# Optimization experiments

Measured on AMD Instinct MI355X. Metric: run time of the kernel, lower is better.

The kernel has to match this reference:

```python
import jax, jax.numpy as jnp
import numpy as np

OUT, IN = 4096, 4096
GROUP_SIZE = 128
NUMEL = OUT * IN                 # 16,777,216 int4 values
N_GROUPS = NUMEL // GROUP_SIZE   # 131,072
N_PACKED = NUMEL // 2            # 8,388,608 bytes (stored as int32 0..255)


def _dequantize_int4(q_packed, q_scales, q_zeros):
    """Unpack two 4-bit values per byte, dequant per group, reshape to (OUT, IN)."""
    low = q_packed & 0xF                     # [N_PACKED]
    high = (q_packed >> 4) & 0xF             # [N_PACKED]
    # interleave: flat[2i] = low nibble, flat[2i+1] = high nibble
    q = jnp.stack([low, high], axis=-1).reshape(NUMEL)            # [NUMEL] int
    qg = q.astype(jnp.float32).reshape(N_GROUPS, GROUP_SIZE)      # [G, group]
    w = (qg - q_zeros[:, None]) * q_scales[:, None]
    return w.reshape(OUT, IN)


def setup_inputs() -> dict:
    key = jax.random.key(0)
    k = jax.random.split(key, 6)
    x = jax.random.normal(k[0], (4, 2048, IN), dtype=jnp.float32)
    q_packed = jax.random.randint(k[1], (N_PACKED,), 0, 256, dtype=jnp.int32)
    q_scales = jax.random.uniform(k[2], (N_GROUPS,), dtype=jnp.float32) * 0.02 + 1e-3
    q_zeros = jax.random.uniform(k[3], (N_GROUPS,), dtype=jnp.float32) * 15.0
    delta_weight = jax.random.normal(k[4], (OUT, IN), dtype=jnp.float32) * 0.01
    bias = jax.random.normal(k[5], (OUT,), dtype=jnp.float32)
    return {"x": x, "q_packed": q_packed, "q_scales": q_scales,
            "q_zeros": q_zeros, "delta_weight": delta_weight, "bias": bias}


def reference(x, q_packed, q_scales, q_zeros, delta_weight, bias):
    W = _dequantize_int4(q_packed, q_scales, q_zeros)   # [OUT, IN]
    W_eff = W + delta_weight
    # F.linear: y = x @ W_eff^T + bias
    h = jnp.einsum('bsi,oi->bso', x, W_eff) + bias
    return h
```

## Files before the change

kernel.cpp:

```cpp
#include <hip/hip_runtime.h>


#define M_DIM 8192
#define N_DIM 4096
#define K_DIM 4096
#define NUMEL (N_DIM * K_DIM)

typedef _Float16 half_t;
typedef __attribute__((ext_vector_type(4))) _Float16 half4v;
typedef __attribute__((ext_vector_type(8))) _Float16 half8v;
typedef __attribute__((ext_vector_type(4))) float float4v;
typedef __attribute__((ext_vector_type(4))) int int4v;

#define KTILES 64
#define LDT 72

static __device__ __forceinline__ void gload16(const void* g, void* l) {
    __builtin_amdgcn_global_load_lds(
        (const __attribute__((address_space(1))) void*)g,
        (__attribute__((address_space(3))) void*)l, 16, 0, 0);
}

__global__ __launch_bounds__(256) void k_pack_w(
    const int* __restrict__ qp, const float* __restrict__ sc,
    const float* __restrict__ zr, const float* __restrict__ dwt,
    unsigned char* __restrict__ Wp)
{
    const size_t o = ((size_t)blockIdx.x * 256 + threadIdx.x) << 4;
    const int chunk16 = (int)(o >> 14);
    const int c  = (int)(o >> 10) & 15;
    const int ln = (int)(o >> 4) & 63;
    const int n = (chunk16 >> 6) * 128 + (c >> 1) * 16 + (ln & 15);
    const int k = (chunk16 & 63) * 64 + (c & 1) * 32 + (ln >> 4) * 8;
    const long flat = (long)n * K_DIM + k;
    const int g = n * 32 + (k >> 7);
    const float s = sc[g];
    const float zs = zr[g] * s;
    int4v q4 = *(const int4v*)(qp + (flat >> 1));
    float4v d0 = *(const float4v*)(dwt + flat);
    float4v d1 = *(const float4v*)(dwt + flat + 4);
    float d[8] = {d0[0], d0[1], d0[2], d0[3], d1[0], d1[1], d1[2], d1[3]};
    half8v vh;
#pragma unroll
    for (int j = 0; j < 4; ++j) {
        vh[2*j]   = (half_t)fmaf((float)(q4[j] & 15),        s, d[2*j]   - zs);
        vh[2*j+1] = (half_t)fmaf((float)((q4[j] >> 4) & 15), s, d[2*j+1] - zs);
    }
    *(half8v*)(Wp + o) = vh;
}

__global__ __launch_bounds__(256) void k_pack_x(
    const float* __restrict__ X, unsigned char* __restrict__ Xp)
{
    const size_t o = ((size_t)blockIdx.x * 256 + threadIdx.x) << 4;
    const int chunk16 = (int)(o >> 14);
    const int c  = (int)(o >> 10) & 15;
    const int ln = (int)(o >> 4) & 63;
    const int m = (chunk16 >> 6) * 128 + (c >> 1) * 16 + (ln & 15);
    const int k = (chunk16 & 63) * 64 + (c & 1) * 32 + (ln >> 4) * 8;
    const float* src = X + (size_t)m * K_DIM + k;
    float4v x0 = *(const float4v*)(src);
    float4v x1 = *(const float4v*)(src + 4);
    half8v vh;
    vh[0] = (half_t)x0[0]; vh[1] = (half_t)x0[1];
    vh[2] = (half_t)x0[2]; vh[3] = (half_t)x0[3];
    vh[4] = (half_t)x1[0]; vh[5] = (half_t)x1[1];
    vh[6] = (half_t)x1[2]; vh[7] = (half_t)x1[3];
    *(half8v*)(Xp + o) = vh;
}

#define BARX() do { __builtin_amdgcn_sched_barrier(0); \
                    __builtin_amdgcn_s_barrier(); \
                    __builtin_amdgcn_sched_barrier(0); } while(0)
#define WAITV0() do { __builtin_amdgcn_sched_barrier(0); \
                      asm volatile("s_waitcnt vmcnt(0)" ::: "memory"); \
                      __builtin_amdgcn_sched_barrier(0); } while(0)

#define STAGE_TILE(BUF, T) do { \
    const int kt_ = (T) >> 1; \
    const size_t ko_ = ((size_t)kt_ << 14) + (((T) & 1) << 10) + choff; \
    gload16(Apk + apan0 + ko_, &lds[BUF][ldsd]); \
    gload16(Apk + apan1 + ko_, &lds[BUF][ldsd + 8192]); \
    gload16(Bpk + bpan0 + ko_, &lds[BUF][ldsd + 16384]); \
    gload16(Bpk + bpan1 + ko_, &lds[BUF][ldsd + 24576]); \
} while(0)

#define RD_A(BUF, DST, RT0) do { \
_Pragma("unroll") for (int i_ = 0; i_ < 4; ++i_) \
        DST[i_] = *(const half8v*)(&lds[BUF][awm + (((RT0) + i_) << 10) + lane16]); \
} while(0)

#define RD_B(BUF, DST) do { \
_Pragma("unroll") for (int j_ = 0; j_ < 4; ++j_) \
        DST[j_] = *(const half8v*)(&lds[BUF][16384 + bq + (j_ << 10) + lane16]); \
} while(0)

#define MFMA16(A0, AR, BR) do { \
    __builtin_amdgcn_s_setprio(1); \
_Pragma("unroll") for (int i_ = 0; i_ < 4; ++i_) \
_Pragma("unroll") for (int j_ = 0; j_ < 4; ++j_) \
        acc[(A0)+i_][j_] = __builtin_amdgcn_mfma_f32_16x16x32_f16( \
            AR[i_], BR[j_], acc[(A0)+i_][j_], 0, 0, 0); \
    __builtin_amdgcn_s_setprio(0); \
} while(0)

#define WINDOW(BA, BB, TA, STG) do { \
    if (STG) { STAGE_TILE((BA)^2, (TA)+2); STAGE_TILE((BB)^2, (TA)+3); } \
    RD_A(BA, ahA, 0); RD_B(BA, bfA); \
    MFMA16(0, ahA, bfA); \
    RD_A(BA, ah2, 4); \
    MFMA16(4, ah2, bfA); \
    RD_A(BB, ahB, 0); RD_B(BB, bfB); \
    MFMA16(0, ahB, bfB); \
    RD_A(BB, ah2, 4); \
    MFMA16(4, ah2, bfB); \
    WAITV0(); BARX(); \
} while(0)

__global__ __launch_bounds__(512, 2) void k_gemm_win(
    const unsigned char* __restrict__ Apk, const unsigned char* __restrict__ Bpk,
    const float* __restrict__ bias, float* __restrict__ Y)
{
    __shared__ __align__(16) unsigned char lds[4][32768];

    const int tid  = threadIdx.x;
    const int lane = tid & 63;
    const int wave = tid >> 6;
    const int wm = wave >> 2;
    const int wn = wave & 3;
    const int awm = wm * 8192;
    const int bq  = (wn >> 1) * 8192 + (wn & 1) * 4096;
    const int lane16 = lane << 4;
    const int ldsd = tid << 4;
    const size_t choff = ((size_t)(tid >> 6) << 11) + ((tid & 63) << 4);

    const int wg = blockIdx.x;
    const int swg = (wg & 7) * 64 + (wg >> 3);
    const int bn = swg & 15;
    const int bm = swg >> 4;

    const size_t apan0 = ((size_t)(2 * bm) * KTILES) << 14;
    const size_t apan1 = ((size_t)(2 * bm + 1) * KTILES) << 14;
    const size_t bpan0 = ((size_t)(2 * bn) * KTILES) << 14;
    const size_t bpan1 = ((size_t)(2 * bn + 1) * KTILES) << 14;

    half8v ahA[4], ahB[4], ah2[4], bfA[4], bfB[4];
    float4v acc[8][4];
    const float4v zero4 = {0.f, 0.f, 0.f, 0.f};
#pragma unroll
    for (int i = 0; i < 8; ++i)
#pragma unroll
        for (int j = 0; j < 4; ++j) acc[i][j] = zero4;

    STAGE_TILE(0, 0); STAGE_TILE(1, 1);
    WAITV0();
    BARX();

    for (int it = 0; it < 31; ++it) {
        const int t = it << 2;
        WINDOW(0, 1, t, 1);
        WINDOW(2, 3, t + 2, 1);
    }
    WINDOW(0, 1, 124, 1);
    WINDOW(2, 3, 126, 0);

    const long m0 = (long)bm * 256 + wm * 128;
    const long n0 = (long)bn * 256 + wn * 64;
#pragma unroll
    for (int mf = 0; mf < 8; ++mf) {
        const long row = m0 + mf * 16 + (lane >> 4) * 4;
#pragma unroll
        for (int nf = 0; nf < 4; ++nf) {
            const long col = n0 + nf * 16 + (lane & 15);
            const float b = bias[col];
#pragma unroll
            for (int r = 0; r < 4; ++r)
                __builtin_nontemporal_store(acc[mf][nf][r] + b,
                                            &Y[(row + r) * N_DIM + col]);
        }
    }
}

__global__ __launch_bounds__(256, 2) void k_gemm_fused(
    const float* __restrict__ X, const int* __restrict__ qp,
    const float* __restrict__ sc, const float* __restrict__ zr,
    const float* __restrict__ dwt,
    const float* __restrict__ bias, float* __restrict__ Y)
{
    __shared__ __align__(16) half_t Ah[128 * LDT];
    __shared__ __align__(16) half_t Bh[128 * LDT];

    const int tid  = threadIdx.x;
    const int lane = tid & 63;
    const int wave = tid >> 6;
    const int wm = wave >> 1, wn = wave & 1;
    const int bn = blockIdx.x & 31;
    const int bm = blockIdx.x >> 5;
    const long m0 = (long)bm * 128;
    const long n0 = (long)bn * 128;
    const int fr = lane & 15;
    const int ko = (lane >> 4) * 8;

    const float4v zero4 = {0.f, 0.f, 0.f, 0.f};
    float4v acc[4][4];
#pragma unroll
    for (int i = 0; i < 4; ++i)
#pragma unroll
        for (int j = 0; j < 4; ++j) acc[i][j] = zero4;

    for (int k0 = 0; k0 < K_DIM; k0 += 64) {
        {
            const int ar = tid >> 4;
            const int ac = (tid & 15) * 4;
#pragma unroll
            for (int rr = 0; rr < 8; ++rr) {
                const int row = ar + rr * 16;
                float4v xv = *(const float4v*)(X + (m0 + row) * K_DIM + k0 + ac);
                half4v h;
#pragma unroll
                for (int j = 0; j < 4; ++j) h[j] = (half_t)xv[j];
                *(half4v*)(Ah + row * LDT + ac) = h;
            }
        }
        {
            const int cr = tid >> 3;
            const int cc = (tid & 7) * 8;
#pragma unroll
            for (int rr = 0; rr < 4; ++rr) {
                const int row = cr + rr * 32;
                const long n = n0 + row;
                const int g = (int)(n * 32 + (k0 >> 7));
                const float s = sc[g];
                const float zs = zr[g] * s;
                const long flat = n * K_DIM + k0 + cc;
                int4v q4 = *(const int4v*)(qp + (flat >> 1));
                float4v d0 = *(const float4v*)(dwt + flat);
                float4v d1 = *(const float4v*)(dwt + flat + 4);
                float d[8] = {d0[0], d0[1], d0[2], d0[3], d1[0], d1[1], d1[2], d1[3]};
                half8v vh;
#pragma unroll
                for (int j = 0; j < 4; ++j) {
                    vh[2*j]   = (half_t)fmaf((float)(q4[j] & 15),        s, d[2*j]   - zs);
                    vh[2*j+1] = (half_t)fmaf((float)((q4[j] >> 4) & 15), s, d[2*j+1] - zs);
                }
                *(half8v*)(Bh + row * LDT + cc) = vh;
            }
        }
        __syncthreads();
#pragma unroll
        for (int ks = 0; ks < 2; ++ks) {
            const int kk = ks * 32 + ko;
            half8v a2[4], b2[4];
#pragma unroll
            for (int i = 0; i < 4; ++i) {
                a2[i] = *(const half8v*)(Ah + (wm * 64 + i * 16 + fr) * LDT + kk);
                b2[i] = *(const half8v*)(Bh + (wn * 64 + i * 16 + fr) * LDT + kk);
            }
#pragma unroll
            for (int i = 0; i < 4; ++i)
#pragma unroll
                for (int j = 0; j < 4; ++j)
                    acc[i][j] = __builtin_amdgcn_mfma_f32_16x16x32_f16(
                        a2[i], b2[j], acc[i][j], 0, 0, 0);
        }
        __syncthreads();
    }

#pragma unroll
    for (int i = 0; i < 4; ++i) {
        const long mrow = m0 + wm * 64 + i * 16 + (lane >> 4) * 4;
#pragma unroll
        for (int j = 0; j < 4; ++j) {
            const long col = n0 + wn * 64 + j * 16 + (lane & 15);
            const float b = bias[col];
#pragma unroll
            for (int r = 0; r < 4; ++r)
                Y[(mrow + r) * N_DIM + col] = acc[i][j][r] + b;
        }
    }
}

extern "C" void kernel_launch(void* const* d_in, const int* in_sizes, int n_in,
                              void* d_out, int out_size, void* d_ws, size_t ws_size,
                              hipStream_t stream)
{
    const float* X  = (const float*)d_in[0];
    const int*   qp = (const int*)d_in[1];
    const float* sc = (const float*)d_in[2];
    const float* zr = (const float*)d_in[3];
    const float* dwt = (const float*)d_in[4];
    const float* bs = (const float*)d_in[5];
    float* Y = (float*)d_out;

    const size_t needB = (size_t)N_DIM * K_DIM * 2;
    const size_t needA = (size_t)M_DIM * K_DIM * 2;

    if (ws_size >= needA + needB) {
        unsigned char* Bpk = (unsigned char*)d_ws;
        unsigned char* Apk = Bpk + needB;
        k_pack_w<<<dim3((unsigned)(needB >> 12)), dim3(256), 0, stream>>>(qp, sc, zr, dwt, Bpk);
        k_pack_x<<<dim3((unsigned)(needA >> 12)), dim3(256), 0, stream>>>(X, Apk);
        k_gemm_win<<<dim3((M_DIM / 256) * (N_DIM / 256)), dim3(512), 0, stream>>>(Apk, Bpk, bs, Y);
    } else {
        k_gemm_fused<<<dim3((M_DIM / 128) * (N_DIM / 128)), dim3(256), 0, stream>>>(
            X, qp, sc, zr, dwt, bs, Y);
    }
}
```

Baseline: 302.4 us.

## Shrink GEMM tile to 128x256 with triple-buffered LDS for higher occupancy

Replaces the 256x256-tile windowed GEMM with a 128x256 tile that uses three 24KB LDS buffers and half the accumulators, launching twice as many workgroups with a target of 4 blocks per CU. The pipeline now issues the next tile's loads after reading fragments and waits with a partial vmcnt, so loads overlap the MFMAs. The smaller tile is meant to lower register and LDS pressure so more waves can hide latency. In exchange each tile reuses A and B less, global traffic per FLOP goes up, and the output stores drop the nontemporal hint.

Result: no change. 305.6 us (+1.1%).

```diff
diff --git a/kernel.cpp b/kernel.cpp
--- a/kernel.cpp
+++ b/kernel.cpp
@@ -72,111 +72,110 @@
 #define BARX() do { __builtin_amdgcn_sched_barrier(0); \
                     __builtin_amdgcn_s_barrier(); \
                     __builtin_amdgcn_sched_barrier(0); } while(0)
-#define WAITV0() do { __builtin_amdgcn_sched_barrier(0); \
-                      asm volatile("s_waitcnt vmcnt(0)" ::: "memory"); \
+#define WAITV(N) do { asm volatile("s_waitcnt vmcnt(" #N ")" ::: "memory"); \
                       __builtin_amdgcn_sched_barrier(0); } while(0)
-
-#define STAGE_TILE(BUF, T) do { \
-    const int kt_ = (T) >> 1; \
-    const size_t ko_ = ((size_t)kt_ << 14) + (((T) & 1) << 10) + choff; \
-    gload16(Apk + apan0 + ko_, &lds[BUF][ldsd]); \
-    gload16(Apk + apan1 + ko_, &lds[BUF][ldsd + 8192]); \
-    gload16(Bpk + bpan0 + ko_, &lds[BUF][ldsd + 16384]); \
-    gload16(Bpk + bpan1 + ko_, &lds[BUF][ldsd + 24576]); \
+#define LGKM0() do { asm volatile("s_waitcnt lgkmcnt(0)" ::: "memory"); \
+                     __builtin_amdgcn_sched_barrier(0); } while(0)
+
+#define STAGE(BUF, T) do { \
+    const size_t ko_ = ((size_t)((T) >> 1) << 14) + (size_t)(((T) & 1) << 10); \
+    gload16(aB + ko_,  &lds[BUF][sdst]); \
+    gload16(bB0 + ko_, &lds[BUF][sdst + 8192]); \
+    gload16(bB1 + ko_, &lds[BUF][sdst + 16384]); \
 } while(0)
 
-#define RD_A(BUF, DST, RT0) do { \
+#define RD_AB(BUF) do { \
 _Pragma("unroll") for (int i_ = 0; i_ < 4; ++i_) \
-        DST[i_] = *(const half8v*)(&lds[BUF][awm + (((RT0) + i_) << 10) + lane16]); \
+        ah[i_] = *(const half8v*)(&lds[BUF][aoff + (i_ << 10)]); \
+_Pragma("unroll") for (int j_ = 0; j_ < 4; ++j_) \
+        bh[j_] = *(const half8v*)(&lds[BUF][boff + (j_ << 10)]); \
 } while(0)
 
-#define RD_B(BUF, DST) do { \
-_Pragma("unroll") for (int j_ = 0; j_ < 4; ++j_) \
-        DST[j_] = *(const half8v*)(&lds[BUF][16384 + bq + (j_ << 10) + lane16]); \
-} while(0)
-
-#define MFMA16(A0, AR, BR) do { \
+#define MFMA16() do { \
     __builtin_amdgcn_s_setprio(1); \
 _Pragma("unroll") for (int i_ = 0; i_ < 4; ++i_) \
 _Pragma("unroll") for (int j_ = 0; j_ < 4; ++j_) \
-        acc[(A0)+i_][j_] = __builtin_amdgcn_mfma_f32_16x16x32_f16( \
-            AR[i_], BR[j_], acc[(A0)+i_][j_], 0, 0, 0); \
+        acc[i_][j_] = __builtin_amdgcn_mfma_f32_16x16x32_f16( \
+            ah[i_], bh[j_], acc[i_][j_], 0, 0, 0); \
     __builtin_amdgcn_s_setprio(0); \
 } while(0)
 
-#define WINDOW(BA, BB, TA, STG) do { \
-    if (STG) { STAGE_TILE((BA)^2, (TA)+2); STAGE_TILE((BB)^2, (TA)+3); } \
-    RD_A(BA, ahA, 0); RD_B(BA, bfA); \
-    MFMA16(0, ahA, bfA); \
-    RD_A(BA, ah2, 4); \
-    MFMA16(4, ah2, bfA); \
-    RD_A(BB, ahB, 0); RD_B(BB, bfB); \
-    MFMA16(0, ahB, bfB); \
-    RD_A(BB, ah2, 4); \
-    MFMA16(4, ah2, bfB); \
-    WAITV0(); BARX(); \
+#define STEP(RB, SB, T) do { \
+    RD_AB(RB); \
+    STAGE(SB, (T) + 2); \
+    WAITV(3); \
+    LGKM0(); \
+    BARX(); \
+    MFMA16(); \
 } while(0)
 
-__global__ __launch_bounds__(512, 2) void k_gemm_win(
+__global__ __launch_bounds__(512, 4) void k_gemm_occ(
     const unsigned char* __restrict__ Apk, const unsigned char* __restrict__ Bpk,
     const float* __restrict__ bias, float* __restrict__ Y)
 {
-    __shared__ __align__(16) unsigned char lds[4][32768];
+    __shared__ __align__(16) unsigned char lds[3][24576];
 
     const int tid  = threadIdx.x;
     const int lane = tid & 63;
     const int wave = tid >> 6;
-    const int wm = wave >> 2;
-    const int wn = wave & 3;
-    const int awm = wm * 8192;
-    const int bq  = (wn >> 1) * 8192 + (wn & 1) * 4096;
+    const int wm2 = wave >> 2;
+    const int wn2 = wave & 3;
     const int lane16 = lane << 4;
-    const int ldsd = tid << 4;
-    const size_t choff = ((size_t)(tid >> 6) << 11) + ((tid & 63) << 4);
+    const int aoff = (wm2 << 12) + lane16;
+    const int boff = 8192 + ((wn2 >> 1) << 13) + ((wn2 & 1) << 12) + lane16;
+    const int sdst = tid << 4;
 
     const int wg = blockIdx.x;
-    const int swg = (wg & 7) * 64 + (wg >> 3);
+    const int swg = (wg & 7) * 128 + (wg >> 3);
     const int bn = swg & 15;
     const int bm = swg >> 4;
 
-    const size_t apan0 = ((size_t)(2 * bm) * KTILES) << 14;
-    const size_t apan1 = ((size_t)(2 * bm + 1) * KTILES) << 14;
-    const size_t bpan0 = ((size_t)(2 * bn) * KTILES) << 14;
-    const size_t bpan1 = ((size_t)(2 * bn + 1) * KTILES) << 14;
-
-    half8v ahA[4], ahB[4], ah2[4], bfA[4], bfB[4];
-    float4v acc[8][4];
+    const size_t thoff = ((size_t)(tid >> 6) << 11) + (size_t)((tid & 63) << 4);
+    const unsigned char* aB  = Apk + ((size_t)bm << 20) + thoff;
+    const unsigned char* bB0 = Bpk + ((size_t)(2 * bn) << 20) + thoff;
+    const unsigned char* bB1 = Bpk + ((size_t)(2 * bn + 1) << 20) + thoff;
+
+    half8v ah[4], bh[4];
+    float4v acc[4][4];
     const float4v zero4 = {0.f, 0.f, 0.f, 0.f};
 #pragma unroll
-    for (int i = 0; i < 8; ++i)
+    for (int i = 0; i < 4; ++i)
 #pragma unroll
         for (int j = 0; j < 4; ++j) acc[i][j] = zero4;
 
-    STAGE_TILE(0, 0); STAGE_TILE(1, 1);
-    WAITV0();
+    STAGE(0, 0);
+    STAGE(1, 1);
+    WAITV(3);
     BARX();
 
-    for (int it = 0; it < 31; ++it) {
-        const int t = it << 2;
-        WINDOW(0, 1, t, 1);
-        WINDOW(2, 3, t + 2, 1);
-    }
-    WINDOW(0, 1, 124, 1);
-    WINDOW(2, 3, 126, 0);
-
-    const long m0 = (long)bm * 256 + wm * 128;
-    const long n0 = (long)bn * 256 + wn * 64;
-#pragma unroll
-    for (int mf = 0; mf < 8; ++mf) {
-        const long row = m0 + mf * 16 + (lane >> 4) * 4;
-#pragma unroll
-        for (int nf = 0; nf < 4; ++nf) {
-            const long col = n0 + nf * 16 + (lane & 15);
+    for (int it = 0; it < 42; ++it) {
+        const int t = it * 3;
+        STEP(0, 2, t);
+        STEP(1, 0, t + 1);
+        STEP(2, 1, t + 2);
+    }
+
+    RD_AB(0);
+    WAITV(0);
+    LGKM0();
+    BARX();
+    MFMA16();
+    RD_AB(1);
+    LGKM0();
+    MFMA16();
+
+    const long m0 = (long)bm * 128 + wm2 * 64;
+    const long n0 = (long)bn * 256 + wn2 * 64;
+#pragma unroll
+    for (int i = 0; i < 4; ++i) {
+        const long row = m0 + i * 16 + (lane >> 4) * 4;
+#pragma unroll
+        for (int j = 0; j < 4; ++j) {
+            const long col = n0 + j * 16 + (lane & 15);
             const float b = bias[col];
 #pragma unroll
             for (int r = 0; r < 4; ++r)
-                __builtin_nontemporal_store(acc[mf][nf][r] + b,
-                                            &Y[(row + r) * N_DIM + col]);
+                Y[(row + r) * N_DIM + col] = acc[i][j][r] + b;
         }
     }
 }
@@ -300,7 +299,7 @@
         unsigned char* Apk = Bpk + needB;
         k_pack_w<<<dim3((unsigned)(needB >> 12)), dim3(256), 0, stream>>>(qp, sc, zr, dwt, Bpk);
         k_pack_x<<<dim3((unsigned)(needA >> 12)), dim3(256), 0, stream>>>(X, Apk);
-        k_gemm_win<<<dim3((M_DIM / 256) * (N_DIM / 256)), dim3(512), 0, stream>>>(Apk, Bpk, bs, Y);
+        k_gemm_occ<<<dim3((M_DIM / 128) * (N_DIM / 256)), dim3(512), 0, stream>>>(Apk, Bpk, bs, Y);
     } else {
         k_gemm_fused<<<dim3((M_DIM / 128) * (N_DIM / 128)), dim3(256), 0, stream>>>(
             X, qp, sc, zr, dwt, bs, Y);
```
